# Kernel tuning notes

Hardware: AMD Instinct MI355X
Metric: run time of the kernel (lower is better)

## Reference

```python
import jax, jax.numpy as jnp
import numpy as np

B, DAYS, N, E = 2, 8, 10000, 80000
C_IN, C_OUT, H = 32, 32, 4
NEG_SLOPE = 0.2


def setup_inputs() -> dict:
    key = jax.random.key(0)
    ks = jax.random.split(key, 7)
    x = jax.random.randint(ks[0], (B, DAYS, N), 0, N)
    adjacency = jax.random.randint(ks[1], (2, E), 0, N)
    embedding = jax.random.normal(ks[2], (N, C_IN), dtype=jnp.float32)
    # GATConv linear: in_channels -> heads*out_channels
    W = jax.random.normal(ks[3], (C_IN, H * C_OUT), dtype=jnp.float32) / np.sqrt(C_IN)
    att_src = jax.random.normal(ks[4], (H, C_OUT), dtype=jnp.float32) / np.sqrt(C_OUT)
    att_dst = jax.random.normal(ks[5], (H, C_OUT), dtype=jnp.float32) / np.sqrt(C_OUT)
    bias = jnp.zeros((H * C_OUT,), dtype=jnp.float32)
    return {"x": x, "adjacency": adjacency, "embedding": embedding,
            "W": W, "att_src": att_src, "att_dst": att_dst, "bias": bias}


def _gat_forward(feat, src, dst, W, att_src, att_dst, bias):
    # feat: [G, N, C_IN]; same edge list shared across the G graphs
    G = feat.shape[0]
    xh = (feat @ W).reshape(G, N, H, C_OUT)              # [G,N,H,C]
    a_src = jnp.einsum('gnhc,hc->gnh', xh, att_src)       # [G,N,H]
    a_dst = jnp.einsum('gnhc,hc->gnh', xh, att_dst)
    alpha = a_src[:, src] + a_dst[:, dst]                 # [G,Et,H]
    alpha = jnp.where(alpha >= 0, alpha, NEG_SLOPE * alpha)

    def per_graph(al, msgs):
        # segment softmax over incoming edges of each dst node
        m = jax.ops.segment_max(al, dst, num_segments=N)  # [N,H]
        e = jnp.exp(al - m[dst])                          # [Et,H]
        s = jax.ops.segment_sum(e, dst, num_segments=N)
        w = e / (s[dst] + 1e-16)
        out = jax.ops.segment_sum(w[..., None] * msgs, dst, num_segments=N)
        return out                                        # [N,H,C]

    out = jax.vmap(per_graph)(alpha, xh[:, src])          # [G,N,H,C]
    return out.reshape(G, N, H * C_OUT) + bias


def reference(x, adjacency, embedding, W, att_src, att_dst, bias):
    Bd, Dd = x.shape[0], x.shape[1]
    feat = embedding[x].reshape(-1, N, C_IN)              # [G,N,C_IN]
    # GATConv default add_self_loops=True
    loops = jnp.arange(N, dtype=adjacency.dtype)
    src = jnp.concatenate([adjacency[0], loops])
    dst = jnp.concatenate([adjacency[1], loops])
    out = _gat_forward(feat, src, dst, W, att_src, att_dst, bias)
    return out.reshape(Bd, Dd, -1)
```

## Files before the change

### kernel.cpp

```cpp
#include <hip/hip_runtime.h>
#include <hip/hip_bf16.h>
#include <math.h>

#define C_IN 32
#define H 4
#define C_OUT 32
#define HC (H * C_OUT)
#define NEG_SLOPE 0.2f
#define CSR_STRIDE 64
#define G_MAX 16

typedef float v2f __attribute__((ext_vector_type(2)));

#define RPB 16
__global__ __launch_bounds__(256) void build_kernel(
        const int* __restrict__ adj, int E, int N,
        int* __restrict__ deg, int* __restrict__ csr,
        const float* __restrict__ emb, const float* __restrict__ W,
        const float* __restrict__ att_src, const float* __restrict__ att_dst,
        __hip_bfloat16* __restrict__ T, float* __restrict__ ta_src,
        float* __restrict__ ta_dst, int tblocks) {
    if ((int)blockIdx.x >= tblocks) {
        int e = (blockIdx.x - tblocks) * 256 + threadIdx.x;
        int Et = E + N;
        if (e < Et) {
            int s = (e < E) ? adj[e] : (e - E);
            int d = (e < E) ? adj[E + e] : (e - E);
            int pos = atomicAdd(&deg[d], 1);
            if (pos < CSR_STRIDE) csr[(d << 6) + pos] = s;
        }
        return;
    }
    int t = threadIdx.x;
    int sub = t >> 7;
    int tc = t & 127;
    int h = tc >> 5, c = tc & 31;
    int base = blockIdx.x * RPB;
    int nmax = (N - base < RPB) ? (N - base) : RPB;

    float wcol[C_IN];
#pragma unroll
    for (int k = 0; k < C_IN; k++) wcol[k] = W[k * HC + tc];
    float as = att_src[h * C_OUT + c];
    float adw = att_dst[h * C_OUT + c];

    for (int it = sub; it < nmax; it += 2) {
        int r = __builtin_amdgcn_readfirstlane(base + it);
        const float* ep = emb + (size_t)r * C_IN;
        float acc = 0.f;
#pragma unroll
        for (int k = 0; k < C_IN; k++) acc += ep[k] * wcol[k];
        T[(size_t)r * HC + tc] = __float2bfloat16(acc);
        float ps = acc * as, pd = acc * adw;
#pragma unroll
        for (int o = 16; o; o >>= 1) {
            ps += __shfl_xor(ps, o, 32);
            pd += __shfl_xor(pd, o, 32);
        }
        if (c == 0) {
            ta_src[r * H + h] = ps;
            ta_dst[r * H + h] = pd;
        }
    }
}

__global__ __launch_bounds__(256) void agg_kernel(
        const int* __restrict__ deg, const int* __restrict__ csr,
        const int* __restrict__ x, const unsigned int* __restrict__ Tu,
        const float* __restrict__ ta_src, const float* __restrict__ ta_dst,
        const float* __restrict__ bias, float* __restrict__ out, int N, int G) {
    int wid = threadIdx.x >> 6;
    int lane = threadIdx.x & 63;
    int n = blockIdx.x * 4 + wid;
    if (n >= N) return;

    int g1 = lane >> 2;
    int h1 = lane & 3;
    int h2 = lane >> 4;
    int gc1 = (g1 < G) ? g1 : (G - 1);

    int dg = deg[n];
    if (dg > CSR_STRIDE) dg = CSR_STRIDE;
    const int* cb = csr + (n << 6);

    int xgn = x[(size_t)gc1 * N + n];
    float ad = ta_dst[xgn * H + h1];

    v2f acc[G_MAX];
    float dsum[G_MAX];
#pragma unroll
    for (int g = 0; g < G_MAX; g++) { acc[g] = (v2f){0.f, 0.f}; dsum[g] = 0.f; }

    for (int c0 = 0; c0 < dg; c0 += 8) {
        int cnt = dg - c0;
        cnt = (cnt > 8) ? 8 : cnt;
        float w_pre[8];
        int xs_pre[8];
#pragma unroll
        for (int e = 0; e < 8; e++) {
            w_pre[e] = 0.f;
            xs_pre[e] = 0;
            if (e < cnt) {
                int s = __builtin_amdgcn_readfirstlane(cb[c0 + e]);
                int xs = x[(size_t)gc1 * N + s];
                xs_pre[e] = xs;
                float a = ta_src[xs * H + h1] + ad;
                a = (a >= 0.f) ? a : NEG_SLOPE * a;
                w_pre[e] = __expf(a);
            }
        }
#pragma unroll
        for (int e = 0; e < 8; e++) {
            if (e >= cnt) break;
#pragma unroll
            for (int g = 0; g < G_MAX; g++) {
                float w = __shfl(w_pre[e], g * 4 + h2, 64);
                int xg = __builtin_amdgcn_readlane(xs_pre[e], g * 4);
                unsigned int u = Tu[(xg << 6) + lane];
                v2f t = {__uint_as_float(u << 16),
                         __uint_as_float(u & 0xffff0000u)};
                acc[g] += (v2f){w, w} * t;
                dsum[g] += w;
            }
        }
    }

    float2 b2 = *(const float2*)(bias + lane * 2);
    size_t obase = (size_t)n * HC + lane * 2;
    for (int g = 0; g < G; g++) {
        float inv = __builtin_amdgcn_rcpf(dsum[g] + 1e-16f);
        float2 o2;
        o2.x = acc[g].x * inv + b2.x;
        o2.y = acc[g].y * inv + b2.y;
        *(float2*)(out + obase + (size_t)g * N * HC) = o2;
    }
}

extern "C" void kernel_launch(void* const* d_in, const int* in_sizes, int n_in,
                              void* d_out, int out_size, void* d_ws, size_t ws_size,
                              hipStream_t stream) {
    const int*   x       = (const int*)d_in[0];
    const int*   adj     = (const int*)d_in[1];
    const float* emb     = (const float*)d_in[2];
    const float* W       = (const float*)d_in[3];
    const float* att_src = (const float*)d_in[4];
    const float* att_dst = (const float*)d_in[5];
    const float* bias    = (const float*)d_in[6];
    float* out = (float*)d_out;

    const int N  = in_sizes[2] / C_IN;
    const int GN = in_sizes[0];
    const int G  = GN / N;
    const int E  = in_sizes[1] / 2;
    const int Et = E + N;

    char* ws = (char*)d_ws;
    size_t o = 0;
    auto carve = [&](size_t bytes) -> void* {
        void* p = ws + o;
        o = (o + bytes + 255) & ~(size_t)255;
        return p;
    };
    __hip_bfloat16* T = (__hip_bfloat16*)carve((size_t)N * HC * sizeof(__hip_bfloat16));
    float* ta_src  = (float*)carve((size_t)N * H * sizeof(float));
    float* ta_dst  = (float*)carve((size_t)N * H * sizeof(float));
    int*   deg     = (int*)carve((size_t)N * sizeof(int));
    int*   csr     = (int*)carve((size_t)N * CSR_STRIDE * sizeof(int));

    hipMemsetAsync(deg, 0, (size_t)N * sizeof(int), stream);

    int tblocks = (N + RPB - 1) / RPB;
    int fblocks = (Et + 255) / 256;
    build_kernel<<<tblocks + fblocks, 256, 0, stream>>>(
        adj, E, N, deg, csr, emb, W, att_src, att_dst, T, ta_src, ta_dst, tblocks);

    agg_kernel<<<(N + 3) / 4, 256, 0, stream>>>(deg, csr, x,
                                                (const unsigned int*)T, ta_src, ta_dst,
                                                bias, out, N, G);
}
```

Measured before the change: 175.0 us.

## Split aggregation work by graph groups across waves instead of one wave per node

The aggregation kernel now launches one block per destination node, and each of its four waves handles four of the sixteen graphs. Each edge's attention weight is computed redundantly per head across lanes, which removes the per-8-edge prefetch and shuffle/readlane staging. Per-wave accumulators shrink from sixteen graphs to four, which lowers register pressure and raises parallelism. In exchange the CSR list and degree are read four times per node and each wave runs a serial gather chain with less latency hiding. The kernel also assumes G is a multiple of four, since a partial group would read out of range.

```diff
diff --git a/kernel.cpp b/kernel.cpp
--- a/kernel.cpp
+++ b/kernel.cpp
@@ -8,7 +8,6 @@
 #define HC (H * C_OUT)
 #define NEG_SLOPE 0.2f
 #define CSR_STRIDE 64
-#define G_MAX 16
 
 typedef float v2f __attribute__((ext_vector_type(2)));
 
@@ -71,68 +70,55 @@
         const float* __restrict__ bias, float* __restrict__ out, int N, int G) {
     int wid = threadIdx.x >> 6;
     int lane = threadIdx.x & 63;
-    int n = blockIdx.x * 4 + wid;
-    if (n >= N) return;
-
-    int g1 = lane >> 2;
-    int h1 = lane & 3;
+    int n = blockIdx.x;
     int h2 = lane >> 4;
-    int gc1 = (g1 < G) ? g1 : (G - 1);
+    int g0 = wid * 4;
+    if (g0 >= G) return;
 
     int dg = deg[n];
     if (dg > CSR_STRIDE) dg = CSR_STRIDE;
     const int* cb = csr + (n << 6);
 
-    int xgn = x[(size_t)gc1 * N + n];
-    float ad = ta_dst[xgn * H + h1];
+    float ad[4];
+    v2f acc[4];
+    float dsum[4];
+#pragma unroll
+    for (int j = 0; j < 4; j++) {
+        int gj = g0 + j;
+        int xgn = __builtin_amdgcn_readfirstlane(x[(size_t)gj * N + n]);
+        ad[j] = ta_dst[xgn * H + h2];
+        acc[j] = (v2f){0.f, 0.f};
+        dsum[j] = 0.f;
+    }
 
-    v2f acc[G_MAX];
-    float dsum[G_MAX];
+#pragma unroll 2
+    for (int e = 0; e < dg; e++) {
+        int s = __builtin_amdgcn_readfirstlane(cb[e]);
+        size_t sbase = (size_t)g0 * N + s;
 #pragma unroll
-    for (int g = 0; g < G_MAX; g++) { acc[g] = (v2f){0.f, 0.f}; dsum[g] = 0.f; }
-
-    for (int c0 = 0; c0 < dg; c0 += 8) {
-        int cnt = dg - c0;
-        cnt = (cnt > 8) ? 8 : cnt;
-        float w_pre[8];
-        int xs_pre[8];
-#pragma unroll
-        for (int e = 0; e < 8; e++) {
-            w_pre[e] = 0.f;
-            xs_pre[e] = 0;
-            if (e < cnt) {
-                int s = __builtin_amdgcn_readfirstlane(cb[c0 + e]);
-                int xs = x[(size_t)gc1 * N + s];
-                xs_pre[e] = xs;
-                float a = ta_src[xs * H + h1] + ad;
-                a = (a >= 0.f) ? a : NEG_SLOPE * a;
-                w_pre[e] = __expf(a);
-            }
-        }
-#pragma unroll
-        for (int e = 0; e < 8; e++) {
-            if (e >= cnt) break;
-#pragma unroll
-            for (int g = 0; g < G_MAX; g++) {
-                float w = __shfl(w_pre[e], g * 4 + h2, 64);
-                int xg = __builtin_amdgcn_readlane(xs_pre[e], g * 4);
-                unsigned int u = Tu[(xg << 6) + lane];
-                v2f t = {__uint_as_float(u << 16),
-                         __uint_as_float(u & 0xffff0000u)};
-                acc[g] += (v2f){w, w} * t;
-                dsum[g] += w;
-            }
+        for (int j = 0; j < 4; j++) {
+            int xs = __builtin_amdgcn_readfirstlane(x[sbase + (size_t)j * N]);
+            float a = ta_src[xs * H + h2] + ad[j];
+            a = fmaxf(a, NEG_SLOPE * a);
+            float w = __expf(a);
+            unsigned int u = Tu[(xs << 6) + lane];
+            v2f t = {__uint_as_float(u << 16),
+                     __uint_as_float(u & 0xffff0000u)};
+            acc[j] += (v2f){w, w} * t;
+            dsum[j] += w;
         }
     }
 
     float2 b2 = *(const float2*)(bias + lane * 2);
     size_t obase = (size_t)n * HC + lane * 2;
-    for (int g = 0; g < G; g++) {
-        float inv = __builtin_amdgcn_rcpf(dsum[g] + 1e-16f);
+#pragma unroll
+    for (int j = 0; j < 4; j++) {
+        int gj = g0 + j;
+        float inv = __builtin_amdgcn_rcpf(dsum[j] + 1e-16f);
         float2 o2;
-        o2.x = acc[g].x * inv + b2.x;
-        o2.y = acc[g].y * inv + b2.y;
-        *(float2*)(out + obase + (size_t)g * N * HC) = o2;
+        o2.x = acc[j].x * inv + b2.x;
+        o2.y = acc[j].y * inv + b2.y;
+        *(float2*)(out + obase + (size_t)gj * N * HC) = o2;
     }
 }
 
@@ -174,7 +160,7 @@
     build_kernel<<<tblocks + fblocks, 256, 0, stream>>>(
         adj, E, N, deg, csr, emb, W, att_src, att_dst, T, ta_src, ta_dst, tblocks);
 
-    agg_kernel<<<(N + 3) / 4, 256, 0, stream>>>(deg, csr, x,
-                                                (const unsigned int*)T, ta_src, ta_dst,
-                                                bias, out, N, G);
+    agg_kernel<<<N, 256, 0, stream>>>(deg, csr, x,
+                                      (const unsigned int*)T, ta_src, ta_dst,
+                                      bias, out, N, G);
 }
```

New measurement: 163.2 us. 6.8% less time.
